# Performance work log

Hardware: AMD Instinct MI355X
Metric: run time of the kernel (lower is better)

Reference implementation:

```python
import jax, jax.numpy as jnp
import numpy as np
from jax import lax

STORAGE = 8
HIDDEN_HEAD = 32
N_BLOCKS = 16


def _conv(x, w, b, padding):
    # x: NCHW, w: OIHW
    y = lax.conv_general_dilated(
        x, w, window_strides=(1, 1), padding=padding,
        dimension_numbers=("NCHW", "OIHW", "NCHW"))
    return y + b[None, :, None, None]


def _min_pool3(x):
    # 3x3 sliding-window min, stride 1, same padding (pad value +inf so it
    return lax.reduce_window(x, float("inf"), lax.min,
                             (1, 1, 3, 3), (1, 1, 1, 1), "SAME")


def setup_inputs() -> dict:
    key = jax.random.key(0)
    ks = jax.random.split(key, 7)
    B, H, W = 8, 512, 512
    x = jax.random.normal(ks[0], (B, 1, H, W), dtype=jnp.float32)
    # initial 1x1 conv: 1 -> 8
    w0 = jax.random.normal(ks[1], (STORAGE, 1, 1, 1), dtype=jnp.float32) * 1.0
    b0 = jax.random.normal(ks[2], (STORAGE,), dtype=jnp.float32) * 0.1
    # head conv 3x3: 8 -> 32
    w1 = jax.random.normal(ks[3], (HIDDEN_HEAD, STORAGE, 3, 3), dtype=jnp.float32) * (1.0 / np.sqrt(STORAGE * 9))
    b1 = jax.random.normal(ks[4], (HIDDEN_HEAD,), dtype=jnp.float32) * 0.1
    # head conv 1x1: 32 -> 1
    w2 = jax.random.normal(ks[5], (1, HIDDEN_HEAD, 1, 1), dtype=jnp.float32) * (1.0 / np.sqrt(HIDDEN_HEAD))
    b2 = jax.random.normal(ks[6], (1,), dtype=jnp.float32) * 0.1
    return {"x": x, "w0": w0, "b0": b0, "w1": w1, "b1": b1, "w2": w2, "b2": b2}


def reference(x, w0, b0, w1, b1, w2, b2):
    h = _conv(x, w0, b0, "SAME")  # [B,8,H,W]
    for _ in range(N_BLOCKS):
        h = h + _min_pool3(h)
    h = _conv(h, w1, b1, "SAME")  # [B,32,H,W]
    h = jax.nn.relu(h)
    return _conv(h, w2, b2, "SAME")  # [B,1,H,W]
```

## Files before the change

### kernel.cpp

```cpp
#include <hip/hip_runtime.h>
#include <math.h>


#define N_PIX (512*512)
#define INF __builtin_inff()

typedef __attribute__((ext_vector_type(2))) float f2;

__device__ __forceinline__ float dpp_shr1(float v, float fill) {
    return __int_as_float(__builtin_amdgcn_update_dpp(
        __float_as_int(fill), __float_as_int(v), 0x138, 0xF, 0xF, false));
}
__device__ __forceinline__ float dpp_shl1(float v, float fill) {
    return __int_as_float(__builtin_amdgcn_update_dpp(
        __float_as_int(fill), __float_as_int(v), 0x130, 0xF, 0xF, false));
}

__global__ void prep_kernel(const float* __restrict__ w0, const float* __restrict__ b0,
                            const float* __restrict__ w1, const float* __restrict__ b1,
                            float* __restrict__ W)
{
    int tid = threadIdx.x;
    if (tid < 288) {
        int oc = tid / 9, k = tid - oc*9;
        float wp = 0.f, wq = 0.f;
        for (int ic = 0; ic < 8; ++ic) {
            float a = w0[ic];
            float w = w1[oc*72 + ic*9 + k];
            if (a > 0.f) wp += w * a;
            else         wq += w * (-a);
        }
        W[(oc*9 + k)*2 + 0] = wp;
        W[(oc*9 + k)*2 + 1] = wq;
        if (k == 0) {
            float beta[9];
            for (int kk = 0; kk < 9; ++kk) {
                float s = 0.f;
                for (int ic = 0; ic < 8; ++ic) s += b0[ic] * w1[oc*72 + ic*9 + kk];
                beta[kk] = 65536.0f * s;
            }
            for (int r = 0; r < 3; ++r) {
                W[576 + oc*4 + r] = beta[r*3] + beta[r*3+1] + beta[r*3+2]
                                  + ((r == 1) ? b1[oc] : 0.f);
                W[704 + oc*4 + r] = beta[r*3 + 0];
                W[832 + oc*4 + r] = beta[r*3 + 2];
            }
        }
    }
}

struct Row8 { float4 a, b; };

__device__ __forceinline__ Row8 row_update8(const Row8 up, const Row8 mid, const Row8 dn)
{
    float4 va, vb;
    va.x = fminf(fminf(up.a.x, mid.a.x), dn.a.x);
    va.y = fminf(fminf(up.a.y, mid.a.y), dn.a.y);
    va.z = fminf(fminf(up.a.z, mid.a.z), dn.a.z);
    va.w = fminf(fminf(up.a.w, mid.a.w), dn.a.w);
    vb.x = fminf(fminf(up.b.x, mid.b.x), dn.b.x);
    vb.y = fminf(fminf(up.b.y, mid.b.y), dn.b.y);
    vb.z = fminf(fminf(up.b.z, mid.b.z), dn.b.z);
    vb.w = fminf(fminf(up.b.w, mid.b.w), dn.b.w);
    float vmL = dpp_shr1(vb.w, INF);
    float vmR = dpp_shl1(va.x, INF);
    float tm1 = fminf(vmL, va.x);
    float t0 = fminf(va.x, va.y), t1 = fminf(va.y, va.z);
    float t2 = fminf(va.z, va.w), t3 = fminf(va.w, vb.x);
    float t4 = fminf(vb.x, vb.y), t5 = fminf(vb.y, vb.z);
    float t6 = fminf(vb.z, vb.w), t7 = fminf(vb.w, vmR);
    Row8 o;
    o.a.x = mid.a.x + fminf(tm1, t0);
    o.a.y = mid.a.y + fminf(t0, t1);
    o.a.z = mid.a.z + fminf(t1, t2);
    o.a.w = mid.a.w + fminf(t2, t3);
    o.b.x = mid.b.x + fminf(t3, t4);
    o.b.y = mid.b.y + fminf(t4, t5);
    o.b.z = mid.b.z + fminf(t5, t6);
    o.b.w = mid.b.w + fminf(t6, t7);
    return o;
}

__global__ __launch_bounds__(512, 2) void erode16_kernel(
    const float* __restrict__ x, float* __restrict__ A)
{
    __shared__ float halo[2][8][2][8][64];
    const int tid   = threadIdx.x;
    const int lane  = tid & 63;
    const int w     = tid >> 6;
    const int ty    = blockIdx.x;
    const int plane = blockIdx.y;
    const int colg  = lane * 8;
    const int row0g = ty*32 - 16 + w*8;

    const float* sp = x + (plane & 7)*N_PIX;
    const float sgn = (plane >= 8) ? -1.f : 1.f;

    Row8 h[8];
    #pragma unroll
    for (int r = 0; r < 8; ++r) {
        int gy = row0g + r;
        if ((unsigned)gy < 512u) {
            const float* rp = sp + gy*512 + colg;
            float4 a = *(const float4*)rp;
            float4 b = *(const float4*)(rp + 4);
            h[r].a = make_float4(a.x*sgn, a.y*sgn, a.z*sgn, a.w*sgn);
            h[r].b = make_float4(b.x*sgn, b.y*sgn, b.z*sgn, b.w*sgn);
        } else {
            h[r].a = make_float4(INF, INF, INF, INF);
            h[r].b = h[r].a;
        }
    }

    const Row8 inf8 = { make_float4(INF,INF,INF,INF), make_float4(INF,INF,INF,INF) };
    for (int s = 0; s < 16; ++s) {
        int par = s & 1;
        {
            float* ht = &halo[par][w][0][0][lane];
            ht[0*64]=h[0].a.x; ht[1*64]=h[0].a.y; ht[2*64]=h[0].a.z; ht[3*64]=h[0].a.w;
            ht[4*64]=h[0].b.x; ht[5*64]=h[0].b.y; ht[6*64]=h[0].b.z; ht[7*64]=h[0].b.w;
            float* hb = &halo[par][w][1][0][lane];
            hb[0*64]=h[7].a.x; hb[1*64]=h[7].a.y; hb[2*64]=h[7].a.z; hb[3*64]=h[7].a.w;
            hb[4*64]=h[7].b.x; hb[5*64]=h[7].b.y; hb[6*64]=h[7].b.z; hb[7*64]=h[7].b.w;
        }
        Row8 o1 = h[1], o6 = h[6];
        Row8 prev = h[0];
        #pragma unroll
        for (int r = 1; r <= 6; ++r) {
            Row8 tmp = h[r];
            h[r] = row_update8(prev, h[r], h[r+1]);
            prev = tmp;
        }
        __syncthreads();
        Row8 up = inf8, dn = inf8;
        if (w > 0) {
            const float* hu = &halo[par][w-1][1][0][lane];
            up.a.x=hu[0*64]; up.a.y=hu[1*64]; up.a.z=hu[2*64]; up.a.w=hu[3*64];
            up.b.x=hu[4*64]; up.b.y=hu[5*64]; up.b.z=hu[6*64]; up.b.w=hu[7*64];
        }
        if (w < 7) {
            const float* hd = &halo[par][w+1][0][0][lane];
            dn.a.x=hd[0*64]; dn.a.y=hd[1*64]; dn.a.z=hd[2*64]; dn.a.w=hd[3*64];
            dn.b.x=hd[4*64]; dn.b.y=hd[5*64]; dn.b.z=hd[6*64]; dn.b.w=hd[7*64];
        }
        h[0] = row_update8(up, h[0], o1);
        h[7] = row_update8(o6, h[7], dn);
    }

    if (w >= 2 && w <= 5) {
        float* dp = A + plane*N_PIX;
        #pragma unroll
        for (int r = 0; r < 8; ++r) {
            float* op = dp + (row0g + r)*512 + colg;
            *(float4*)op       = h[r].a;
            *(float4*)(op + 4) = h[r].b;
        }
    }
}

__global__ __launch_bounds__(256) void head_kernel(
    const float* __restrict__ A, const float* __restrict__ W,
    const float* __restrict__ w2, const float* __restrict__ b2,
    float* __restrict__ out)
{
    const int tid  = threadIdx.x;
    const int lane = tid & 63;
    const int w    = tid >> 6;
    const int img  = blockIdx.x >> 7;
    const int y    = (blockIdx.x & 127)*4 + w;
    const int x0   = lane*8;

    const float* P = A + img*N_PIX;
    const float* Q = A + (8 + img)*N_PIX;

    f2 pq[3][10];
    #pragma unroll
    for (int dy = 0; dy < 3; ++dy) {
        int gy = y + dy - 1;
        if ((unsigned)gy < 512u) {
            const float* rp = P + gy*512 + x0;
            const float* rq = Q + gy*512 + x0;
            float4 a = *(const float4*)rp;
            float4 b = *(const float4*)(rp + 4);
            float4 c = *(const float4*)rq;
            float4 d = *(const float4*)(rq + 4);
            pq[dy][1] = (f2){a.x, c.x}; pq[dy][2] = (f2){a.y, c.y};
            pq[dy][3] = (f2){a.z, c.z}; pq[dy][4] = (f2){a.w, c.w};
            pq[dy][5] = (f2){b.x, d.x}; pq[dy][6] = (f2){b.y, d.y};
            pq[dy][7] = (f2){b.z, d.z}; pq[dy][8] = (f2){b.w, d.w};
            pq[dy][0] = (f2){dpp_shr1(b.w, 0.f), dpp_shr1(d.w, 0.f)};
            pq[dy][9] = (f2){dpp_shl1(a.x, 0.f), dpp_shl1(c.x, 0.f)};
        } else {
            #pragma unroll
            for (int j = 0; j < 10; ++j) pq[dy][j] = (f2){0.f, 0.f};
        }
    }

    const float ry0 = (y >= 1)   ? 1.f : 0.f;
    const float ry2 = (y <= 510) ? 1.f : 0.f;
    const float mL  = (lane == 0)  ? -1.f : 0.f;
    const float mR  = (lane == 63) ? -1.f : 0.f;

    float o[8];
    #pragma unroll
    for (int j = 0; j < 8; ++j) o[j] = 0.f;

    const f2* Wv = (const f2*)W;
    #pragma unroll 2
    for (int oc = 0; oc < 32; ++oc) {
        f2 acc[8];
        {
            f2 wv0 = Wv[oc*9];
            #pragma unroll
            for (int j = 0; j < 8; ++j) acc[j] = wv0 * pq[0][j];
        }
        #pragma unroll
        for (int t = 1; t < 9; ++t) {
            const int ky = t / 3, kx = t - ky*3;
            f2 wv = Wv[oc*9 + t];
            #pragma unroll
            for (int j = 0; j < 8; ++j) acc[j] += wv * pq[ky][kx + j];
        }
        float base = W[576 + oc*4 + 1]
                   + ry0 * W[576 + oc*4 + 0]
                   + ry2 * W[576 + oc*4 + 2];
        float cl = W[704 + oc*4 + 1] + ry0 * W[704 + oc*4 + 0] + ry2 * W[704 + oc*4 + 2];
        float cr = W[832 + oc*4 + 1] + ry0 * W[832 + oc*4 + 0] + ry2 * W[832 + oc*4 + 2];
        float s[8];
        #pragma unroll
        for (int j = 0; j < 8; ++j) s[j] = acc[j].x + acc[j].y + base;
        s[0] = fmaf(cl, mL, s[0]);
        s[7] = fmaf(cr, mR, s[7]);
        float sc = w2[oc];
        #pragma unroll
        for (int j = 0; j < 8; ++j) o[j] += fmaxf(s[j], 0.f) * sc;
    }

    float bb = b2[0];
    float* op = out + img*N_PIX + y*512 + x0;
    *(float4*)(op)     = make_float4(o[0]+bb, o[1]+bb, o[2]+bb, o[3]+bb);
    *(float4*)(op + 4) = make_float4(o[4]+bb, o[5]+bb, o[6]+bb, o[7]+bb);
}

extern "C" void kernel_launch(void* const* d_in, const int* in_sizes, int n_in,
                              void* d_out, int out_size, void* d_ws, size_t ws_size,
                              hipStream_t stream) {
    const float* x  = (const float*)d_in[0];
    const float* w0 = (const float*)d_in[1];
    const float* b0 = (const float*)d_in[2];
    const float* w1 = (const float*)d_in[3];
    const float* b1 = (const float*)d_in[4];
    const float* w2 = (const float*)d_in[5];
    const float* b2 = (const float*)d_in[6];
    float* out = (float*)d_out;

    float* wsf = (float*)d_ws;
    float* A = wsf;
    float* W = wsf + 16*N_PIX;

    prep_kernel<<<1, 320, 0, stream>>>(w0, b0, w1, b1, W);

    dim3 eg(16, 16);
    erode16_kernel<<<eg, 512, 0, stream>>>(x, A);

    head_kernel<<<1024, 256, 0, stream>>>(A, W, w2, b2, out);
}
```

Baseline: 129.7 us.

## Exchange two-row halos to run two erosion steps per barrier; fold prep into erode

The erosion loop now swaps two boundary rows per side through shared memory and advances two erosion steps per iteration. This halves the number of __syncthreads barriers and LDS round trips, at the cost of a few redundant row updates per wave. The weight-prep kernel is also merged into the first erode block, which removes one kernel launch. The shared halo buffer doubles in size.

Result: no change. 128.3 us (-1.0%).

```diff
diff --git a/kernel.cpp b/kernel.cpp
--- a/kernel.cpp
+++ b/kernel.cpp
@@ -14,39 +14,6 @@
 __device__ __forceinline__ float dpp_shl1(float v, float fill) {
     return __int_as_float(__builtin_amdgcn_update_dpp(
         __float_as_int(fill), __float_as_int(v), 0x130, 0xF, 0xF, false));
-}
-
-__global__ void prep_kernel(const float* __restrict__ w0, const float* __restrict__ b0,
-                            const float* __restrict__ w1, const float* __restrict__ b1,
-                            float* __restrict__ W)
-{
-    int tid = threadIdx.x;
-    if (tid < 288) {
-        int oc = tid / 9, k = tid - oc*9;
-        float wp = 0.f, wq = 0.f;
-        for (int ic = 0; ic < 8; ++ic) {
-            float a = w0[ic];
-            float w = w1[oc*72 + ic*9 + k];
-            if (a > 0.f) wp += w * a;
-            else         wq += w * (-a);
-        }
-        W[(oc*9 + k)*2 + 0] = wp;
-        W[(oc*9 + k)*2 + 1] = wq;
-        if (k == 0) {
-            float beta[9];
-            for (int kk = 0; kk < 9; ++kk) {
-                float s = 0.f;
-                for (int ic = 0; ic < 8; ++ic) s += b0[ic] * w1[oc*72 + ic*9 + kk];
-                beta[kk] = 65536.0f * s;
-            }
-            for (int r = 0; r < 3; ++r) {
-                W[576 + oc*4 + r] = beta[r*3] + beta[r*3+1] + beta[r*3+2]
-                                  + ((r == 1) ? b1[oc] : 0.f);
-                W[704 + oc*4 + r] = beta[r*3 + 0];
-                W[832 + oc*4 + r] = beta[r*3 + 2];
-            }
-        }
-    }
 }
 
 struct Row8 { float4 a, b; };
@@ -81,10 +48,52 @@
     return o;
 }
 
+__device__ __forceinline__ void halo_write(float* hp, const Row8& v) {
+    hp[0*64]=v.a.x; hp[1*64]=v.a.y; hp[2*64]=v.a.z; hp[3*64]=v.a.w;
+    hp[4*64]=v.b.x; hp[5*64]=v.b.y; hp[6*64]=v.b.z; hp[7*64]=v.b.w;
+}
+__device__ __forceinline__ Row8 halo_read(const float* hp) {
+    Row8 v;
+    v.a.x=hp[0*64]; v.a.y=hp[1*64]; v.a.z=hp[2*64]; v.a.w=hp[3*64];
+    v.b.x=hp[4*64]; v.b.y=hp[5*64]; v.b.z=hp[6*64]; v.b.w=hp[7*64];
+    return v;
+}
+
 __global__ __launch_bounds__(512, 2) void erode16_kernel(
-    const float* __restrict__ x, float* __restrict__ A)
+    const float* __restrict__ x, float* __restrict__ A,
+    const float* __restrict__ w0, const float* __restrict__ b0,
+    const float* __restrict__ w1, const float* __restrict__ b1,
+    float* __restrict__ W)
 {
-    __shared__ float halo[2][8][2][8][64];
+    if (blockIdx.x == 0 && blockIdx.y == 0 && threadIdx.x < 288) {
+        int tid = threadIdx.x;
+        int oc = tid / 9, k = tid - oc*9;
+        float wp = 0.f, wq = 0.f;
+        for (int ic = 0; ic < 8; ++ic) {
+            float a = w0[ic];
+            float w = w1[oc*72 + ic*9 + k];
+            if (a > 0.f) wp += w * a;
+            else         wq += w * (-a);
+        }
+        W[(oc*9 + k)*2 + 0] = wp;
+        W[(oc*9 + k)*2 + 1] = wq;
+        if (k == 0) {
+            float beta[9];
+            for (int kk = 0; kk < 9; ++kk) {
+                float s = 0.f;
+                for (int ic = 0; ic < 8; ++ic) s += b0[ic] * w1[oc*72 + ic*9 + kk];
+                beta[kk] = 65536.0f * s;
+            }
+            for (int r = 0; r < 3; ++r) {
+                W[576 + oc*4 + r] = beta[r*3] + beta[r*3+1] + beta[r*3+2]
+                                  + ((r == 1) ? b1[oc] : 0.f);
+                W[704 + oc*4 + r] = beta[r*3 + 0];
+                W[832 + oc*4 + r] = beta[r*3 + 2];
+            }
+        }
+    }
+
+    __shared__ float halo[2][8][4][8][64];
     const int tid   = threadIdx.x;
     const int lane  = tid & 63;
     const int w     = tid >> 6;
@@ -113,38 +122,40 @@
     }
 
     const Row8 inf8 = { make_float4(INF,INF,INF,INF), make_float4(INF,INF,INF,INF) };
-    for (int s = 0; s < 16; ++s) {
+    for (int s = 0; s < 8; ++s) {
         int par = s & 1;
-        {
-            float* ht = &halo[par][w][0][0][lane];
-            ht[0*64]=h[0].a.x; ht[1*64]=h[0].a.y; ht[2*64]=h[0].a.z; ht[3*64]=h[0].a.w;
-            ht[4*64]=h[0].b.x; ht[5*64]=h[0].b.y; ht[6*64]=h[0].b.z; ht[7*64]=h[0].b.w;
-            float* hb = &halo[par][w][1][0][lane];
-            hb[0*64]=h[7].a.x; hb[1*64]=h[7].a.y; hb[2*64]=h[7].a.z; hb[3*64]=h[7].a.w;
-            hb[4*64]=h[7].b.x; hb[5*64]=h[7].b.y; hb[6*64]=h[7].b.z; hb[7*64]=h[7].b.w;
-        }
-        Row8 o1 = h[1], o6 = h[6];
-        Row8 prev = h[0];
-        #pragma unroll
-        for (int r = 1; r <= 6; ++r) {
-            Row8 tmp = h[r];
-            h[r] = row_update8(prev, h[r], h[r+1]);
-            prev = tmp;
-        }
+        halo_write(&halo[par][w][0][0][lane], h[0]);
+        halo_write(&halo[par][w][1][0][lane], h[1]);
+        halo_write(&halo[par][w][2][0][lane], h[6]);
+        halo_write(&halo[par][w][3][0][lane], h[7]);
+        Row8 n2 = row_update8(h[1], h[2], h[3]);
+        Row8 n3 = row_update8(h[2], h[3], h[4]);
+        Row8 n4 = row_update8(h[3], h[4], h[5]);
+        Row8 n5 = row_update8(h[4], h[5], h[6]);
         __syncthreads();
-        Row8 up = inf8, dn = inf8;
+        Row8 um2 = inf8, um1 = inf8, dp0 = inf8, dp1 = inf8;
         if (w > 0) {
-            const float* hu = &halo[par][w-1][1][0][lane];
-            up.a.x=hu[0*64]; up.a.y=hu[1*64]; up.a.z=hu[2*64]; up.a.w=hu[3*64];
-            up.b.x=hu[4*64]; up.b.y=hu[5*64]; up.b.z=hu[6*64]; up.b.w=hu[7*64];
+            um2 = halo_read(&halo[par][w-1][2][0][lane]);
+            um1 = halo_read(&halo[par][w-1][3][0][lane]);
         }
         if (w < 7) {
-            const float* hd = &halo[par][w+1][0][0][lane];
-            dn.a.x=hd[0*64]; dn.a.y=hd[1*64]; dn.a.z=hd[2*64]; dn.a.w=hd[3*64];
-            dn.b.x=hd[4*64]; dn.b.y=hd[5*64]; dn.b.z=hd[6*64]; dn.b.w=hd[7*64];
-        }
-        h[0] = row_update8(up, h[0], o1);
-        h[7] = row_update8(o6, h[7], dn);
+            dp0 = halo_read(&halo[par][w+1][0][0][lane]);
+            dp1 = halo_read(&halo[par][w+1][1][0][lane]);
+        }
+        Row8 nm1 = row_update8(um2, um1, h[0]);
+        Row8 n0  = row_update8(um1, h[0], h[1]);
+        Row8 n1  = row_update8(h[0], h[1], h[2]);
+        Row8 n6  = row_update8(h[5], h[6], h[7]);
+        Row8 n7  = row_update8(h[6], h[7], dp0);
+        Row8 n8  = row_update8(h[7], dp0, dp1);
+        h[0] = row_update8(nm1, n0, n1);
+        h[1] = row_update8(n0,  n1, n2);
+        h[2] = row_update8(n1,  n2, n3);
+        h[3] = row_update8(n2,  n3, n4);
+        h[4] = row_update8(n3,  n4, n5);
+        h[5] = row_update8(n4,  n5, n6);
+        h[6] = row_update8(n5,  n6, n7);
+        h[7] = row_update8(n6,  n7, n8);
     }
 
     if (w >= 2 && w <= 5) {
@@ -258,10 +269,8 @@
     float* A = wsf;
     float* W = wsf + 16*N_PIX;
 
-    prep_kernel<<<1, 320, 0, stream>>>(w0, b0, w1, b1, W);
-
     dim3 eg(16, 16);
-    erode16_kernel<<<eg, 512, 0, stream>>>(x, A);
+    erode16_kernel<<<eg, 512, 0, stream>>>(x, A, w0, b0, w1, b1, W);
 
     head_kernel<<<1024, 256, 0, stream>>>(A, W, w2, b2, out);
 }
```

## Give each erosion wave 16 rows, halve block size, fold prep into erode

Applied to the files above, without the earlier changes.

Each wavefront now holds 16 rows in registers instead of 8, and a block has 4 waves of 256 threads instead of 8 waves of 512. Fewer waves per block means less halo traffic through LDS per row, and halo accesses now use paired f2 loads and stores. The weight-prep kernel is merged into block (0,0) of the erode kernel, removing one launch. In exchange, register pressure roughly doubles (16 Row8 values per thread), the launch bounds drop to one block per CU, and only 256 blocks of 4 waves are launched, which lowers occupancy and latency hiding.

Measured after the change: 130.8 us. Within noise of the previous version (+0.9%).

```diff
diff --git a/kernel.cpp b/kernel.cpp
--- a/kernel.cpp
+++ b/kernel.cpp
@@ -14,39 +14,6 @@
 __device__ __forceinline__ float dpp_shl1(float v, float fill) {
     return __int_as_float(__builtin_amdgcn_update_dpp(
         __float_as_int(fill), __float_as_int(v), 0x130, 0xF, 0xF, false));
-}
-
-__global__ void prep_kernel(const float* __restrict__ w0, const float* __restrict__ b0,
-                            const float* __restrict__ w1, const float* __restrict__ b1,
-                            float* __restrict__ W)
-{
-    int tid = threadIdx.x;
-    if (tid < 288) {
-        int oc = tid / 9, k = tid - oc*9;
-        float wp = 0.f, wq = 0.f;
-        for (int ic = 0; ic < 8; ++ic) {
-            float a = w0[ic];
-            float w = w1[oc*72 + ic*9 + k];
-            if (a > 0.f) wp += w * a;
-            else         wq += w * (-a);
-        }
-        W[(oc*9 + k)*2 + 0] = wp;
-        W[(oc*9 + k)*2 + 1] = wq;
-        if (k == 0) {
-            float beta[9];
-            for (int kk = 0; kk < 9; ++kk) {
-                float s = 0.f;
-                for (int ic = 0; ic < 8; ++ic) s += b0[ic] * w1[oc*72 + ic*9 + kk];
-                beta[kk] = 65536.0f * s;
-            }
-            for (int r = 0; r < 3; ++r) {
-                W[576 + oc*4 + r] = beta[r*3] + beta[r*3+1] + beta[r*3+2]
-                                  + ((r == 1) ? b1[oc] : 0.f);
-                W[704 + oc*4 + r] = beta[r*3 + 0];
-                W[832 + oc*4 + r] = beta[r*3 + 2];
-            }
-        }
-    }
 }
 
 struct Row8 { float4 a, b; };
@@ -81,24 +48,70 @@
     return o;
 }
 
-__global__ __launch_bounds__(512, 2) void erode16_kernel(
-    const float* __restrict__ x, float* __restrict__ A)
+__device__ __forceinline__ void halo_write(f2* hp, const Row8& v) {
+    hp[0*64] = (f2){v.a.x, v.a.y};
+    hp[1*64] = (f2){v.a.z, v.a.w};
+    hp[2*64] = (f2){v.b.x, v.b.y};
+    hp[3*64] = (f2){v.b.z, v.b.w};
+}
+__device__ __forceinline__ Row8 halo_read(const f2* hp) {
+    f2 p0 = hp[0*64], p1 = hp[1*64], p2 = hp[2*64], p3 = hp[3*64];
+    Row8 v;
+    v.a = make_float4(p0.x, p0.y, p1.x, p1.y);
+    v.b = make_float4(p2.x, p2.y, p3.x, p3.y);
+    return v;
+}
+
+__global__ __launch_bounds__(256, 1) void erode16_kernel(
+    const float* __restrict__ x, float* __restrict__ A,
+    const float* __restrict__ w0, const float* __restrict__ b0,
+    const float* __restrict__ w1, const float* __restrict__ b1,
+    float* __restrict__ W)
 {
-    __shared__ float halo[2][8][2][8][64];
+    if (blockIdx.x == 0 && blockIdx.y == 0) {
+        for (int t = threadIdx.x; t < 288; t += 256) {
+            int oc = t / 9, k = t - oc*9;
+            float wp = 0.f, wq = 0.f;
+            for (int ic = 0; ic < 8; ++ic) {
+                float a = w0[ic];
+                float w = w1[oc*72 + ic*9 + k];
+                if (a > 0.f) wp += w * a;
+                else         wq += w * (-a);
+            }
+            W[(oc*9 + k)*2 + 0] = wp;
+            W[(oc*9 + k)*2 + 1] = wq;
+            if (k == 0) {
+                float beta[9];
+                for (int kk = 0; kk < 9; ++kk) {
+                    float s = 0.f;
+                    for (int ic = 0; ic < 8; ++ic) s += b0[ic] * w1[oc*72 + ic*9 + kk];
+                    beta[kk] = 65536.0f * s;
+                }
+                for (int r = 0; r < 3; ++r) {
+                    W[576 + oc*4 + r] = beta[r*3] + beta[r*3+1] + beta[r*3+2]
+                                      + ((r == 1) ? b1[oc] : 0.f);
+                    W[704 + oc*4 + r] = beta[r*3 + 0];
+                    W[832 + oc*4 + r] = beta[r*3 + 2];
+                }
+            }
+        }
+    }
+
+    __shared__ f2 halo[2][4][2][4][64];
     const int tid   = threadIdx.x;
     const int lane  = tid & 63;
     const int w     = tid >> 6;
     const int ty    = blockIdx.x;
     const int plane = blockIdx.y;
     const int colg  = lane * 8;
-    const int row0g = ty*32 - 16 + w*8;
+    const int row0g = ty*32 - 16 + w*16;
 
     const float* sp = x + (plane & 7)*N_PIX;
     const float sgn = (plane >= 8) ? -1.f : 1.f;
 
-    Row8 h[8];
+    Row8 h[16];
     #pragma unroll
-    for (int r = 0; r < 8; ++r) {
+    for (int r = 0; r < 16; ++r) {
         int gy = row0g + r;
         if ((unsigned)gy < 512u) {
             const float* rp = sp + gy*512 + colg;
@@ -115,42 +128,28 @@
     const Row8 inf8 = { make_float4(INF,INF,INF,INF), make_float4(INF,INF,INF,INF) };
     for (int s = 0; s < 16; ++s) {
         int par = s & 1;
-        {
-            float* ht = &halo[par][w][0][0][lane];
-            ht[0*64]=h[0].a.x; ht[1*64]=h[0].a.y; ht[2*64]=h[0].a.z; ht[3*64]=h[0].a.w;
-            ht[4*64]=h[0].b.x; ht[5*64]=h[0].b.y; ht[6*64]=h[0].b.z; ht[7*64]=h[0].b.w;
-            float* hb = &halo[par][w][1][0][lane];
-            hb[0*64]=h[7].a.x; hb[1*64]=h[7].a.y; hb[2*64]=h[7].a.z; hb[3*64]=h[7].a.w;
-            hb[4*64]=h[7].b.x; hb[5*64]=h[7].b.y; hb[6*64]=h[7].b.z; hb[7*64]=h[7].b.w;
-        }
-        Row8 o1 = h[1], o6 = h[6];
+        halo_write(&halo[par][w][0][0][lane], h[0]);
+        halo_write(&halo[par][w][1][0][lane], h[15]);
+        Row8 o1 = h[1];
         Row8 prev = h[0];
         #pragma unroll
-        for (int r = 1; r <= 6; ++r) {
+        for (int r = 1; r <= 14; ++r) {
             Row8 tmp = h[r];
             h[r] = row_update8(prev, h[r], h[r+1]);
             prev = tmp;
         }
         __syncthreads();
         Row8 up = inf8, dn = inf8;
-        if (w > 0) {
-            const float* hu = &halo[par][w-1][1][0][lane];
-            up.a.x=hu[0*64]; up.a.y=hu[1*64]; up.a.z=hu[2*64]; up.a.w=hu[3*64];
-            up.b.x=hu[4*64]; up.b.y=hu[5*64]; up.b.z=hu[6*64]; up.b.w=hu[7*64];
-        }
-        if (w < 7) {
-            const float* hd = &halo[par][w+1][0][0][lane];
-            dn.a.x=hd[0*64]; dn.a.y=hd[1*64]; dn.a.z=hd[2*64]; dn.a.w=hd[3*64];
-            dn.b.x=hd[4*64]; dn.b.y=hd[5*64]; dn.b.z=hd[6*64]; dn.b.w=hd[7*64];
-        }
-        h[0] = row_update8(up, h[0], o1);
-        h[7] = row_update8(o6, h[7], dn);
-    }
-
-    if (w >= 2 && w <= 5) {
+        if (w > 0) up = halo_read(&halo[par][w-1][1][0][lane]);
+        if (w < 3) dn = halo_read(&halo[par][w+1][0][0][lane]);
+        h[0]  = row_update8(up,   h[0],  o1);
+        h[15] = row_update8(prev, h[15], dn);
+    }
+
+    if (w == 1 || w == 2) {
         float* dp = A + plane*N_PIX;
         #pragma unroll
-        for (int r = 0; r < 8; ++r) {
+        for (int r = 0; r < 16; ++r) {
             float* op = dp + (row0g + r)*512 + colg;
             *(float4*)op       = h[r].a;
             *(float4*)(op + 4) = h[r].b;
@@ -258,10 +257,8 @@
     float* A = wsf;
     float* W = wsf + 16*N_PIX;
 
-    prep_kernel<<<1, 320, 0, stream>>>(w0, b0, w1, b1, W);
-
     dim3 eg(16, 16);
-    erode16_kernel<<<eg, 512, 0, stream>>>(x, A);
+    erode16_kernel<<<eg, 256, 0, stream>>>(x, A, w0, b0, w1, b1, W);
 
     head_kernel<<<1024, 256, 0, stream>>>(A, W, w2, b2, out);
 }
```
